# Kernel optimization log

Measured on AMD Instinct MI355X. Metric: run time of the kernel, lower is better.

Reference implementation:

```python
import jax, jax.numpy as jnp
import numpy as np

MARGIN = 0.3
POS_THRESH_M = 25.0
NEG_THRESH_M = 100.0
EARTH_R = 6371000.0
B, D = 1024, 256


def _pairwise_haversine(gps):
    # gps: [B,2] degrees -> [B,B] meters
    lat = jnp.deg2rad(gps[:, 0])
    dlat = jnp.deg2rad(gps[None, :, 0] - gps[:, None, 0])
    dlon = jnp.deg2rad(gps[None, :, 1] - gps[:, None, 1])
    a = jnp.sin(dlat / 2) ** 2 + jnp.cos(lat)[:, None] * jnp.cos(lat)[None, :] * jnp.sin(dlon / 2) ** 2
    return EARTH_R * 2.0 * jnp.arctan2(jnp.sqrt(a), jnp.sqrt(1.0 - a))


def _pairwise_euclidean(emb):
    # faithful to torch.norm(emb[None]-emb[:,None], dim=-1), with safe sqrt at 0
    diff = emb[None, :, :] - emb[:, None, :]          # [B,B,D]
    sq = jnp.sum(diff * diff, axis=-1)                # [B,B]
    return jnp.where(sq > 0, jnp.sqrt(jnp.where(sq > 0, sq, 1.0)), 0.0)


def setup_inputs() -> dict:
    key = jax.random.key(0)
    k1, k2 = jax.random.split(key)
    embeddings = jax.random.normal(k1, (B, D), dtype=jnp.float32)
    # small geographic box (~222 m x ~182 m) so both positive (<25 m) and
    # negative (>100 m) pairs exist for nearly every anchor
    base = jnp.array([35.0, 139.0], dtype=jnp.float32)
    gps_coords = base + jax.random.uniform(k2, (B, 2), dtype=jnp.float32) * 0.002
    return {"embeddings": embeddings, "gps_coords": gps_coords}


def reference(embeddings, gps_coords):
    n = embeddings.shape[0]
    gps_d = _pairwise_haversine(gps_coords)           # [B,B]
    emb_d = _pairwise_euclidean(embeddings)           # [B,B]
    eye = jnp.eye(n, dtype=bool)
    pos_mask = (gps_d < POS_THRESH_M) & ~eye
    neg_mask = gps_d > NEG_THRESH_M

    has_pos = jnp.any(pos_mask, axis=1)
    has_neg = jnp.any(neg_mask, axis=1)
    valid = has_pos & has_neg                         # anchors contributing a triplet

    # hardest positive per anchor (masked max)
    d_ap = jnp.max(jnp.where(pos_mask, emb_d, -1.0), axis=1)          # [B]

    # semi-hard negatives: d_ap < d < d_ap + margin among negatives
    semi_mask = neg_mask & (emb_d > d_ap[:, None]) & (emb_d < d_ap[:, None] + MARGIN)
    has_semi = jnp.any(semi_mask, axis=1)
    BIG = jnp.float32(1e9)
    semi_min = jnp.min(jnp.where(semi_mask, emb_d, BIG), axis=1)
    neg_min = jnp.min(jnp.where(neg_mask, emb_d, BIG), axis=1)        # fallback: hardest negative
    d_an = jnp.where(has_semi, semi_min, neg_min)

    triplet = jax.nn.relu(d_ap - d_an + MARGIN)
    triplet = jnp.where(valid, triplet, 0.0)
    n_triplets = jnp.sum(valid.astype(jnp.float32))
    loss = jnp.sum(triplet) / jnp.maximum(n_triplets, 1.0)
    return loss
```

## Files before the change

### kernel.cpp

```cpp
#include <hip/hip_runtime.h>

#define NB 1024
#define ND 256
#define APB 8
#define JCH 256
#define NTHR 256
#define MARGINF 0.3f
#define BIGV 1e9f
#define D2R 0.017453292519943295f
#define HD2R 0.008726646259971648f

#define A_POS 3.8495040e-12f
#define A_NEG 6.1592064e-11f

__device__ __forceinline__ float d4(float4 a, float4 b, float acc) {
    return fmaf(a.x,b.x, fmaf(a.y,b.y, fmaf(a.z,b.z, fmaf(a.w,b.w, acc))));
}

__device__ __forceinline__ float reduce8(const float v[8], int lane) {
    const bool b0 = lane & 1, b1 = lane & 2, b2 = lane & 4;
    float n1[4];
    #pragma unroll
    for (int i = 0; i < 4; ++i) {
        float sv = b0 ? v[i]   : v[4+i];
        float kp = b0 ? v[4+i] : v[i];
        n1[i] = kp + __shfl_xor(sv, 1);
    }
    float n2[2];
    #pragma unroll
    for (int i = 0; i < 2; ++i) {
        float sv = b1 ? n1[i]   : n1[2+i];
        float kp = b1 ? n1[2+i] : n1[i];
        n2[i] = kp + __shfl_xor(sv, 2);
    }
    float sv = b2 ? n2[0] : n2[1];
    float kp = b2 ? n2[1] : n2[0];
    float n3 = kp + __shfl_xor(sv, 4);
    return n3 + __shfl_xor(n3, 8);
}

__global__ __launch_bounds__(NTHR, 2) void gram_kernel(
    const float* __restrict__ emb, const float* __restrict__ gps,
    float* __restrict__ sEnc, float* __restrict__ pP)
{
    __shared__ float sPm[4][APB];

    const int tid  = threadIdx.x;
    const int lane = tid & 63;
    const int w    = tid >> 6;
    const int jj   = lane >> 4;
    const int kk   = lane & 15;
    const int ig   = blockIdx.x >> 2;
    const int c    = blockIdx.x & 3;
    const int i0   = ig * APB;
    const int jbase = c * JCH;
    const int a    = 4*(lane & 1) + 2*((lane >> 1) & 1) + ((lane >> 2) & 1);
    const float4* __restrict__ emb4 = (const float4*)emb;

    float4 cA[APB][4];
    #pragma unroll
    for (int ai = 0; ai < APB; ++ai)
        #pragma unroll
        for (int q = 0; q < 4; ++q)
            cA[ai][q] = emb4[(size_t)(i0+ai)*64 + kk + 16*q];

    float sp[APB];
    #pragma unroll
    for (int ai = 0; ai < APB; ++ai) {
        float s = 0.f;
        #pragma unroll
        for (int q = 0; q < 4; ++q) s = d4(cA[ai][q], cA[ai][q], s);
        sp[ai] = s;
    }
    const float SA = reduce8(sp, lane);

    const float latA = gps[2*(i0+a)];
    const float lonA = gps[2*(i0+a)+1];
    const float cosA = cosf(latA * D2R);

    float pmax = -1.f;

    int j = jbase + w*4 + jj;
    float4 v0 = emb4[(size_t)j*64 + kk],      v1 = emb4[(size_t)j*64 + kk+16],
           v2 = emb4[(size_t)j*64 + kk+32],   v3 = emb4[(size_t)j*64 + kk+48];

    #pragma unroll 2
    for (int t = 0; t < 16; ++t) {
        float4 w0, w1, w2, w3;
        if (t < 15) {
            const int jn = jbase + (t+1)*16 + w*4 + jj;
            w0 = emb4[(size_t)jn*64 + kk];    w1 = emb4[(size_t)jn*64 + kk+16];
            w2 = emb4[(size_t)jn*64 + kk+32]; w3 = emb4[(size_t)jn*64 + kk+48];
        }
        float sq = d4(v3,v3, d4(v2,v2, d4(v1,v1, d4(v0,v0, 0.f))));
        float ac[APB];
        #pragma unroll
        for (int ai = 0; ai < APB; ++ai)
            ac[ai] = d4(v3, cA[ai][3], d4(v2, cA[ai][2], d4(v1, cA[ai][1], d4(v0, cA[ai][0], 0.f))));
        #pragma unroll
        for (int off = 1; off < 16; off <<= 1) sq += __shfl_xor(sq, off);
        const float dot = reduce8(ac, lane);

        float d2v = SA + sq - 2.f*dot;
        d2v = d2v > 0.f ? d2v : 0.f;

        const float2 gj = ((const float2*)gps)[j];
        const float cj  = cosf(gj.x * D2R);
        const float sla = sinf((gj.x - latA) * HD2R);
        const float slo = sinf((gj.y - lonA) * HD2R);
        const float hav = fmaf(sla, sla, (cosA*cj) * (slo*slo));
        const bool pos = (hav < A_POS) && (j != i0 + a);
        const bool neg = (hav > A_NEG);

        pmax = fmaxf(pmax, pos ? d2v : -1.f);
        if (!(lane & 8))
            sEnc[(size_t)(i0+a)*NB + j] = neg ? d2v : BIGV;

        j = jbase + (t+1)*16 + w*4 + jj;
        v0 = w0; v1 = w1; v2 = w2; v3 = w3;
    }

    #pragma unroll
    for (int off = 8; off < 64; off <<= 1) pmax = fmaxf(pmax, __shfl_xor(pmax, off));
    if (lane < 8) sPm[w][a] = pmax;
    __syncthreads();
    if (tid < 32) {
        float x = sPm[tid >> 3][tid & 7];
        x = fmaxf(x, __shfl_xor(x, 8));
        x = fmaxf(x, __shfl_xor(x, 16));
        if (tid < 8) pP[(i0 + tid)*4 + c] = x;
    }
}

__global__ __launch_bounds__(256) void rows_kernel(
    const float* __restrict__ sEnc, const float* __restrict__ pP,
    float* __restrict__ tri, float* __restrict__ val)
{
    const int tid = threadIdx.x, lane = tid & 63, w = tid >> 6;
    const int i = blockIdx.x*4 + w;

    const float dap2 = fmaxf(fmaxf(pP[i*4+0], pP[i*4+1]), fmaxf(pP[i*4+2], pP[i*4+3]));
    const bool has_pos = dap2 > -0.5f;
    float lo2 = -1.f, hi2 = -1.f;
    if (has_pos) { const float hb = sqrtf(dap2) + MARGINF; lo2 = dap2; hi2 = hb*hb; }

    float nmin = BIGV, smin = BIGV;
    const float4* __restrict__ row = (const float4*)sEnc + (size_t)i*256;
    #pragma unroll
    for (int p = 0; p < 4; ++p) {
        const float4 x = row[p*64 + lane];
        #pragma unroll
        for (int q = 0; q < 4; ++q) {
            const float xc = (q==0) ? x.x : (q==1) ? x.y : (q==2) ? x.z : x.w;
            nmin = fminf(nmin, xc);
            smin = fminf(smin, (xc > lo2 && xc < hi2) ? xc : BIGV);
        }
    }
    #pragma unroll
    for (int off = 1; off < 64; off <<= 1) {
        nmin = fminf(nmin, __shfl_xor(nmin, off));
        smin = fminf(smin, __shfl_xor(smin, off));
    }
    if (lane == 0) {
        const bool has_neg  = nmin < 0.5f*BIGV;
        const bool has_semi = smin < 0.5f*BIGV;
        const float dan2 = has_semi ? smin : nmin;
        const float dap  = has_pos ? sqrtf(dap2) : 0.f;
        float t = dap - sqrtf(dan2) + MARGINF;
        t = t > 0.f ? t : 0.f;
        const bool valid = has_pos && has_neg;
        tri[i] = valid ? t : 0.f;
        val[i] = valid ? 1.f : 0.f;
    }
}

__global__ __launch_bounds__(256) void finalize_kernel(
    const float* __restrict__ tri, const float* __restrict__ val, float* __restrict__ out)
{
    const int tid = threadIdx.x;
    float st = 0.f, sv = 0.f;
    #pragma unroll
    for (int g = 0; g < 4; ++g) { st += tri[tid + (g<<8)]; sv += val[tid + (g<<8)]; }
    #pragma unroll
    for (int off = 1; off < 64; off <<= 1) { st += __shfl_xor(st, off); sv += __shfl_xor(sv, off); }
    __shared__ float rt[4], rv[4];
    if ((tid & 63) == 0) { rt[tid>>6] = st; rv[tid>>6] = sv; }
    __syncthreads();
    if (tid == 0) {
        float t = rt[0]+rt[1]+rt[2]+rt[3];
        float v = rv[0]+rv[1]+rv[2]+rv[3];
        out[0] = t / fmaxf(v, 1.f);
    }
}

extern "C" void kernel_launch(void* const* d_in, const int* in_sizes, int n_in,
                              void* d_out, int out_size, void* d_ws, size_t ws_size,
                              hipStream_t stream) {
    const float* emb = (const float*)d_in[0];
    const float* gps = (const float*)d_in[1];
    float* ws = (float*)d_ws;

    float* sEnc = ws;
    float* pP   = ws + 1048576;
    float* tri  = pP + 4096;
    float* val  = tri + 1024;

    gram_kernel<<<512, NTHR, 0, stream>>>(emb, gps, sEnc, pP);
    rows_kernel<<<256, 256, 0, stream>>>(sEnc, pP, tri, val);
    finalize_kernel<<<1, 256, 0, stream>>>(tri, val, (float*)d_out);
}
```

Before: 29.35 us.

## Precompute row norms and GPS terms in a prep kernel; split anchors across waves

Adds a prep kernel that computes each row's squared norm, GPS coordinates and cos(lat) once into a float4 table. The gram kernel then reads these per-column values instead of recomputing the norm reduction and cosine per tile. The gram kernel's work split also changes: each wave now handles 4 anchors with 8 lanes per row and 8 float4 per lane, which shortens the shuffle reductions. The cost is an extra kernel launch, more registers for the per-lane vectors, and redundant column loads across wave pairs.

```diff
diff --git a/kernel.cpp b/kernel.cpp
--- a/kernel.cpp
+++ b/kernel.cpp
@@ -17,30 +17,42 @@
     return fmaf(a.x,b.x, fmaf(a.y,b.y, fmaf(a.z,b.z, fmaf(a.w,b.w, acc))));
 }
 
-__device__ __forceinline__ float reduce8(const float v[8], int lane) {
-    const bool b0 = lane & 1, b1 = lane & 2, b2 = lane & 4;
-    float n1[4];
-    #pragma unroll
-    for (int i = 0; i < 4; ++i) {
-        float sv = b0 ? v[i]   : v[4+i];
-        float kp = b0 ? v[4+i] : v[i];
+__device__ __forceinline__ float reduce4(const float v[4], int lane) {
+    const bool b0 = lane & 1, b1 = lane & 2;
+    float n1[2];
+    #pragma unroll
+    for (int i = 0; i < 2; ++i) {
+        float sv = b0 ? v[i]   : v[2+i];
+        float kp = b0 ? v[2+i] : v[i];
         n1[i] = kp + __shfl_xor(sv, 1);
     }
-    float n2[2];
-    #pragma unroll
-    for (int i = 0; i < 2; ++i) {
-        float sv = b1 ? n1[i]   : n1[2+i];
-        float kp = b1 ? n1[2+i] : n1[i];
-        n2[i] = kp + __shfl_xor(sv, 2);
-    }
-    float sv = b2 ? n2[0] : n2[1];
-    float kp = b2 ? n2[1] : n2[0];
-    float n3 = kp + __shfl_xor(sv, 4);
-    return n3 + __shfl_xor(n3, 8);
+    float sv = b1 ? n1[0] : n1[1];
+    float kp = b1 ? n1[1] : n1[0];
+    float n2 = kp + __shfl_xor(sv, 2);
+    return n2 + __shfl_xor(n2, 4);
+}
+
+__global__ __launch_bounds__(256) void prep_kernel(
+    const float* __restrict__ emb, const float* __restrict__ gps,
+    float4* __restrict__ prep)
+{
+    const int tid = threadIdx.x;
+    const int row = blockIdx.x*16 + (tid >> 4);
+    const int kk  = tid & 15;
+    const float4* r4 = (const float4*)emb + (size_t)row*64;
+    float s = 0.f;
+    #pragma unroll
+    for (int c = 0; c < 4; ++c) { float4 v = r4[kk + 16*c]; s = d4(v, v, s); }
+    #pragma unroll
+    for (int off = 1; off < 16; off <<= 1) s += __shfl_xor(s, off);
+    if (kk == 0) {
+        float2 g = ((const float2*)gps)[row];
+        prep[row] = make_float4(s, g.x, g.y, cosf(g.x * D2R));
+    }
 }
 
 __global__ __launch_bounds__(NTHR, 2) void gram_kernel(
-    const float* __restrict__ emb, const float* __restrict__ gps,
+    const float* __restrict__ emb, const float4* __restrict__ prep,
     float* __restrict__ sEnc, float* __restrict__ pP)
 {
     __shared__ float sPm[4][APB];
@@ -48,87 +60,78 @@
     const int tid  = threadIdx.x;
     const int lane = tid & 63;
     const int w    = tid >> 6;
-    const int jj   = lane >> 4;
-    const int kk   = lane & 15;
+    const int jj   = lane >> 3;
+    const int kk   = lane & 7;
+    const int ah   = (w >> 1) * 4;
+    const int a    = ah + 2*(lane & 1) + ((lane >> 1) & 1);
     const int ig   = blockIdx.x >> 2;
     const int c    = blockIdx.x & 3;
     const int i0   = ig * APB;
     const int jbase = c * JCH;
-    const int a    = 4*(lane & 1) + 2*((lane >> 1) & 1) + ((lane >> 2) & 1);
     const float4* __restrict__ emb4 = (const float4*)emb;
 
-    float4 cA[APB][4];
-    #pragma unroll
-    for (int ai = 0; ai < APB; ++ai)
-        #pragma unroll
-        for (int q = 0; q < 4; ++q)
-            cA[ai][q] = emb4[(size_t)(i0+ai)*64 + kk + 16*q];
-
-    float sp[APB];
-    #pragma unroll
-    for (int ai = 0; ai < APB; ++ai) {
-        float s = 0.f;
-        #pragma unroll
-        for (int q = 0; q < 4; ++q) s = d4(cA[ai][q], cA[ai][q], s);
-        sp[ai] = s;
-    }
-    const float SA = reduce8(sp, lane);
-
-    const float latA = gps[2*(i0+a)];
-    const float lonA = gps[2*(i0+a)+1];
-    const float cosA = cosf(latA * D2R);
+    float4 cA[4][8];
+    #pragma unroll
+    for (int ai = 0; ai < 4; ++ai)
+        #pragma unroll
+        for (int q = 0; q < 8; ++q)
+            cA[ai][q] = emb4[(size_t)(i0+ah+ai)*64 + kk + 8*q];
+
+    const float4 pa = prep[i0 + a];
+    const float SA = pa.x, latA = pa.y, lonA = pa.z, cosA = pa.w;
 
     float pmax = -1.f;
 
-    int j = jbase + w*4 + jj;
-    float4 v0 = emb4[(size_t)j*64 + kk],      v1 = emb4[(size_t)j*64 + kk+16],
-           v2 = emb4[(size_t)j*64 + kk+32],   v3 = emb4[(size_t)j*64 + kk+48];
+    int jr = jbase + (w & 1)*8 + jj;
+    float4 v[8];
+    #pragma unroll
+    for (int q = 0; q < 8; ++q) v[q] = emb4[(size_t)jr*64 + kk + 8*q];
+    float4 pv = prep[jr];
 
     #pragma unroll 2
     for (int t = 0; t < 16; ++t) {
-        float4 w0, w1, w2, w3;
+        float4 wv[8]; float4 pw;
+        int jr2 = jbase + (t+1)*16 + (w & 1)*8 + jj;
         if (t < 15) {
-            const int jn = jbase + (t+1)*16 + w*4 + jj;
-            w0 = emb4[(size_t)jn*64 + kk];    w1 = emb4[(size_t)jn*64 + kk+16];
-            w2 = emb4[(size_t)jn*64 + kk+32]; w3 = emb4[(size_t)jn*64 + kk+48];
+            #pragma unroll
+            for (int q = 0; q < 8; ++q) wv[q] = emb4[(size_t)jr2*64 + kk + 8*q];
+            pw = prep[jr2];
         }
-        float sq = d4(v3,v3, d4(v2,v2, d4(v1,v1, d4(v0,v0, 0.f))));
-        float ac[APB];
-        #pragma unroll
-        for (int ai = 0; ai < APB; ++ai)
-            ac[ai] = d4(v3, cA[ai][3], d4(v2, cA[ai][2], d4(v1, cA[ai][1], d4(v0, cA[ai][0], 0.f))));
-        #pragma unroll
-        for (int off = 1; off < 16; off <<= 1) sq += __shfl_xor(sq, off);
-        const float dot = reduce8(ac, lane);
-
-        float d2v = SA + sq - 2.f*dot;
+        float ac[4];
+        #pragma unroll
+        for (int ai = 0; ai < 4; ++ai) {
+            float s = 0.f;
+            #pragma unroll
+            for (int q = 0; q < 8; ++q) s = d4(v[q], cA[ai][q], s);
+            ac[ai] = s;
+        }
+        const float dot = reduce4(ac, lane);
+
+        float d2v = SA + pv.x - 2.f*dot;
         d2v = d2v > 0.f ? d2v : 0.f;
 
-        const float2 gj = ((const float2*)gps)[j];
-        const float cj  = cosf(gj.x * D2R);
-        const float sla = sinf((gj.x - latA) * HD2R);
-        const float slo = sinf((gj.y - lonA) * HD2R);
-        const float hav = fmaf(sla, sla, (cosA*cj) * (slo*slo));
-        const bool pos = (hav < A_POS) && (j != i0 + a);
+        const float sla = sinf((pv.y - latA) * HD2R);
+        const float slo = sinf((pv.z - lonA) * HD2R);
+        const float hav = fmaf(sla, sla, (cosA * pv.w) * (slo*slo));
+        const bool pos = (hav < A_POS) && (jr != i0 + a);
         const bool neg = (hav > A_NEG);
 
         pmax = fmaxf(pmax, pos ? d2v : -1.f);
-        if (!(lane & 8))
-            sEnc[(size_t)(i0+a)*NB + j] = neg ? d2v : BIGV;
-
-        j = jbase + (t+1)*16 + w*4 + jj;
-        v0 = w0; v1 = w1; v2 = w2; v3 = w3;
-    }
-
-    #pragma unroll
-    for (int off = 8; off < 64; off <<= 1) pmax = fmaxf(pmax, __shfl_xor(pmax, off));
-    if (lane < 8) sPm[w][a] = pmax;
+        if (!(lane & 4))
+            sEnc[(size_t)(i0+a)*NB + jr] = neg ? d2v : BIGV;
+
+        jr = jr2; pv = pw;
+        #pragma unroll
+        for (int q = 0; q < 8; ++q) v[q] = wv[q];
+    }
+
+    #pragma unroll
+    for (int off = 4; off < 64; off <<= 1) pmax = fmaxf(pmax, __shfl_xor(pmax, off));
+    if (lane < 4) sPm[w][a] = pmax;
     __syncthreads();
-    if (tid < 32) {
-        float x = sPm[tid >> 3][tid & 7];
-        x = fmaxf(x, __shfl_xor(x, 8));
-        x = fmaxf(x, __shfl_xor(x, 16));
-        if (tid < 8) pP[(i0 + tid)*4 + c] = x;
+    if (tid < 8) {
+        const int w0 = (tid < 4) ? 0 : 2;
+        pP[(i0 + tid)*4 + c] = fmaxf(sPm[w0][tid], sPm[w0+1][tid]);
     }
 }
 
@@ -200,12 +203,14 @@
     const float* gps = (const float*)d_in[1];
     float* ws = (float*)d_ws;
 
-    float* sEnc = ws;
-    float* pP   = ws + 1048576;
-    float* tri  = pP + 4096;
-    float* val  = tri + 1024;
-
-    gram_kernel<<<512, NTHR, 0, stream>>>(emb, gps, sEnc, pP);
+    float*  sEnc = ws;
+    float4* prep = (float4*)(ws + 1048576);
+    float*  pP   = ws + 1048576 + 4096;
+    float*  tri  = pP + 4096;
+    float*  val  = tri + 1024;
+
+    prep_kernel<<<64, 256, 0, stream>>>(emb, gps, prep);
+    gram_kernel<<<512, NTHR, 0, stream>>>(emb, prep, sEnc, pP);
     rows_kernel<<<256, 256, 0, stream>>>(sEnc, pP, tri, val);
     finalize_kernel<<<1, 256, 0, stream>>>(tri, val, (float*)d_out);
 }
```

Measured after the change: 32.62 us. 1.11x slower.
